# Kernel optimization log

Hardware: AMD Instinct MI355X
Metric: run time of the kernel (lower is better)

## Reference

```python
import jax, jax.numpy as jnp
import numpy as np

I, H, O = 8, 32, 1  # input_size, hidden_size, output_size


def setup_inputs() -> dict:
    key = jax.random.key(0)
    ks = jax.random.split(key, 7)
    B, T = 4096, 256
    s_ih = 1.0 / np.sqrt(H)
    inp = {
        "x": jax.random.normal(ks[0], (B, T, I), dtype=jnp.float32),
        # PyTorch nn.LSTM params, gate order [i, f, g, o]
        "W_ih": jax.random.uniform(ks[1], (4 * H, I), minval=-s_ih, maxval=s_ih, dtype=jnp.float32),
        "W_hh": jax.random.uniform(ks[2], (4 * H, H), minval=-s_ih, maxval=s_ih, dtype=jnp.float32),
        "b_ih": jax.random.uniform(ks[3], (4 * H,), minval=-s_ih, maxval=s_ih, dtype=jnp.float32),
        "b_hh": jax.random.uniform(ks[4], (4 * H,), minval=-s_ih, maxval=s_ih, dtype=jnp.float32),
        # nn.Linear(H, O)
        "W_out": jax.random.uniform(ks[5], (O, H), minval=-s_ih, maxval=s_ih, dtype=jnp.float32),
        "b_out": jax.random.uniform(ks[6], (O,), minval=-s_ih, maxval=s_ih, dtype=jnp.float32),
    }
    return inp


def _lstm_last_h(x, W_ih, W_hh, b_ih, b_hh):
    B = x.shape[0]
    # Precompute input projections for all steps: [T, B, 4H]
    x_proj = jnp.einsum("bti,gi->tbg", x, W_ih) + (b_ih + b_hh)
    h0 = jnp.zeros((B, H), dtype=x.dtype)
    c0 = jnp.zeros((B, H), dtype=x.dtype)

    def step(carry, xp):
        h, c = carry
        z = xp + h @ W_hh.T  # [B, 4H]
        i = jax.nn.sigmoid(z[:, 0 * H:1 * H])
        f = jax.nn.sigmoid(z[:, 1 * H:2 * H])
        g = jnp.tanh(z[:, 2 * H:3 * H])
        o = jax.nn.sigmoid(z[:, 3 * H:4 * H])
        c = f * c + i * g
        h = o * jnp.tanh(c)
        return (h, c), None

    (hT, _), _ = jax.lax.scan(step, (h0, c0), x_proj)
    return hT  # equals out[:, -1, :] for unidirectional batch_first LSTM


def reference(x, W_ih, W_hh, b_ih, b_hh, W_out, b_out):
    hT = _lstm_last_h(x, W_ih, W_hh, b_ih, b_hh)
    return hT @ W_out.T + b_out  # [B, O]
```

## Files before the change

### kernel.cpp

```cpp
#include <hip/hip_runtime.h>


#define T_LEN   256
#define HALF_T  128
#define XSTRIDE 130
#define LOG2E   1.4426950408889634f

typedef short bf16x8 __attribute__((ext_vector_type(8)));
typedef float f32x4  __attribute__((ext_vector_type(4)));
typedef unsigned u32x4 __attribute__((ext_vector_type(4)));

static __device__ inline short f2bf_rne(float f) {
    union { float f; unsigned u; } v; v.f = f;
    unsigned u = v.u;
    return (short)((u + 0x7FFFu + ((u >> 16) & 1u)) >> 16);
}
static __device__ inline unsigned pack_bf2(float a, float b) {
    union { float f; unsigned u; } x, y; x.f = a; y.f = b;
    return ((x.u + 0x8000u) >> 16) | ((y.u + 0x8000u) & 0xFFFF0000u);
}
static __device__ inline float bf2f(short s) {
    union { unsigned u; float f; } v;
    v.u = ((unsigned)(unsigned short)s) << 16;
    return v.f;
}

__global__ __launch_bounds__(256) void lstm_kernel(
    const float* __restrict__ x, const float* __restrict__ W_ih,
    const float* __restrict__ W_hh, const float* __restrict__ b_ih,
    const float* __restrict__ b_hh, const float* __restrict__ W_out,
    const float* __restrict__ b_out, float* __restrict__ out)
{
    __shared__ __attribute__((aligned(16))) short xl[HALF_T * XSTRIDE];
    __shared__ __attribute__((aligned(16))) short h_lds[2][16 * 40];

    const int tid  = threadIdx.x;
    const int w    = tid >> 6;
    const int lane = tid & 63;
    const int L    = lane & 15;
    const int q    = lane >> 4;
    const int row0 = blockIdx.x * 16;
    const float4* xv = (const float4*)x;

    bf16x8 whh[2], wih[2];
    f32x4  bias[2];
#pragma unroll
    for (int e = 0; e < 2; ++e) {
        const int   n = 32 * (L & 3) + 8 * (L >> 2) + 2 * w + e;
        const float s = ((L & 3) == 2 ? 2.f * LOG2E : LOG2E);
        const float* src = W_hh + n * 32 + q * 8;
        bf16x8 fr;
#pragma unroll
        for (int j = 0; j < 8; ++j) fr[j] = f2bf_rne(src[j] * s);
        whh[e] = fr;
        bf16x8 gr = (bf16x8){0,0,0,0,0,0,0,0};
        if (q == 0) {
            const float* s2 = W_ih + n * 8;
#pragma unroll
            for (int j = 0; j < 8; ++j) gr[j] = f2bf_rne(s2[j] * s);
        }
        wih[e] = gr;
        f32x4 bb;
#pragma unroll
        for (int r = 0; r < 4; ++r) {
            const int   nr = 32 * r + 8 * q + 2 * w + e;
            const float sr = (r == 2 ? 2.f * LOG2E : LOG2E);
            bb[r] = (b_ih[nr] + b_hh[nr]) * sr;
        }
        bias[e] = bb;
    }

    for (int i = tid; i < 16 * 40; i += 256) h_lds[0][i] = 0;

#pragma unroll
    for (int it = 0; it < 8; ++it) {
        const int idx = tid + (it << 8);
        const int L2  = idx >> 7;
        const int tl  = idx & (HALF_T - 1);
        const float4* srcp = xv + ((size_t)(row0 + L2) * T_LEN + tl) * 2;
        const float4 a = srcp[0], b = srcp[1];
        u32x4 u;
        u[0] = pack_bf2(a.x, a.y); u[1] = pack_bf2(a.z, a.w);
        u[2] = pack_bf2(b.x, b.y); u[3] = pack_bf2(b.z, b.w);
        *(u32x4*)(&xl[tl * XSTRIDE + L2 * 8]) = u;
    }
    __syncthreads();

    f32x4 zx[2];
    {
        const bf16x8 xf0 = *(const bf16x8*)(&xl[L * 8]);
        zx[0] = __builtin_amdgcn_mfma_f32_16x16x32_bf16(wih[0], xf0, bias[0], 0, 0, 0);
        zx[1] = __builtin_amdgcn_mfma_f32_16x16x32_bf16(wih[1], xf0, bias[1], 0, 0, 0);
    }

    float c0 = 0.f, c1 = 0.f;

#pragma unroll 2
    for (int t = 0; t < T_LEN; ++t) {
        if (t == HALF_T - 1) {
#pragma unroll
            for (int it = 0; it < 8; ++it) {
                const int idx = tid + (it << 8);
                const int L2  = idx >> 7;
                const int tl  = idx & (HALF_T - 1);
                const float4* srcp = xv + ((size_t)(row0 + L2) * T_LEN + HALF_T + tl) * 2;
                const float4 a = srcp[0], b = srcp[1];
                u32x4 u;
                u[0] = pack_bf2(a.x, a.y); u[1] = pack_bf2(a.z, a.w);
                u[2] = pack_bf2(b.x, b.y); u[3] = pack_bf2(b.z, b.w);
                *(u32x4*)(&xl[tl * XSTRIDE + L2 * 8]) = u;
            }
            __syncthreads();
        }

        const int par = t & 1, nxt = par ^ 1;

        const bf16x8 hfrag = *(const bf16x8*)(&h_lds[par][L * 40 + q * 8]);
        int tn = t + 1; if (tn >= T_LEN) tn = T_LEN - 1;
        const bf16x8 xfrag = *(const bf16x8*)(&xl[(tn & (HALF_T - 1)) * XSTRIDE + L * 8]);

        const f32x4 a0 = __builtin_amdgcn_mfma_f32_16x16x32_bf16(whh[0], hfrag, zx[0], 0, 0, 0);
        const f32x4 a1 = __builtin_amdgcn_mfma_f32_16x16x32_bf16(whh[1], hfrag, zx[1], 0, 0, 0);
        zx[0] = __builtin_amdgcn_mfma_f32_16x16x32_bf16(wih[0], xfrag, bias[0], 0, 0, 0);
        zx[1] = __builtin_amdgcn_mfma_f32_16x16x32_bf16(wih[1], xfrag, bias[1], 0, 0, 0);

        float h0, h1;
        {
            const float ei = __builtin_amdgcn_exp2f(-a0[0]);
            const float ef = __builtin_amdgcn_exp2f(-a0[1]);
            const float eg = __builtin_amdgcn_exp2f(-a0[2]);
            const float eo = __builtin_amdgcn_exp2f(-a0[3]);
            const float fv = __builtin_amdgcn_rcpf(1.f + ef);
            const float ig = (1.f - eg) * __builtin_amdgcn_rcpf((1.f + ei) * (1.f + eg));
            c0 = fmaf(fv, c0, ig);
            const float ec = __builtin_amdgcn_exp2f(fminf(c0 * (-2.f * LOG2E), 40.f));
            h0 = (1.f - ec) * __builtin_amdgcn_rcpf((1.f + eo) * (1.f + ec));
        }
        {
            const float ei = __builtin_amdgcn_exp2f(-a1[0]);
            const float ef = __builtin_amdgcn_exp2f(-a1[1]);
            const float eg = __builtin_amdgcn_exp2f(-a1[2]);
            const float eo = __builtin_amdgcn_exp2f(-a1[3]);
            const float fv = __builtin_amdgcn_rcpf(1.f + ef);
            const float ig = (1.f - eg) * __builtin_amdgcn_rcpf((1.f + ei) * (1.f + eg));
            c1 = fmaf(fv, c1, ig);
            const float ec = __builtin_amdgcn_exp2f(fminf(c1 * (-2.f * LOG2E), 40.f));
            h1 = (1.f - ec) * __builtin_amdgcn_rcpf((1.f + eo) * (1.f + ec));
        }

        *(unsigned*)(&h_lds[nxt][L * 40 + 8 * q + 2 * w]) = pack_bf2(h0, h1);

        __syncthreads();
    }

    if (tid < 16) {
        float s = b_out[0];
#pragma unroll
        for (int k = 0; k < 32; ++k) s = fmaf(bf2f(h_lds[0][tid * 40 + k]), W_out[k], s);
        out[row0 + tid] = s;
    }
}

extern "C" void kernel_launch(void* const* d_in, const int* in_sizes, int n_in,
                              void* d_out, int out_size, void* d_ws, size_t ws_size,
                              hipStream_t stream) {
    const float* x     = (const float*)d_in[0];
    const float* W_ih  = (const float*)d_in[1];
    const float* W_hh  = (const float*)d_in[2];
    const float* b_ih  = (const float*)d_in[3];
    const float* b_hh  = (const float*)d_in[4];
    const float* W_out = (const float*)d_in[5];
    const float* b_out = (const float*)d_in[6];
    float* out = (float*)d_out;

    const int B = in_sizes[0] / (T_LEN * 8);
    const int tiles = B / 16;
    lstm_kernel<<<tiles, 256, 0, stream>>>(x, W_ih, W_hh, b_ih, b_hh, W_out, b_out, out);
}
```

Baseline: 147.8 us.

## Run each batch tile on a single wave with register-resident hidden state

Collapses the four-wave block into one 64-lane wave that computes all 128 gate rows via eight MFMAs per step. The MFMA output layout is reused directly as the next step's hidden-state operand, removing the per-step LDS round trip and block barrier. Input x is streamed from global memory with a small register prefetch ring instead of being staged in LDS. The trade-off is four times more serial gate arithmetic per wave and lower occupancy per CU.

```diff
diff --git a/kernel.cpp b/kernel.cpp
--- a/kernel.cpp
+++ b/kernel.cpp
@@ -1,10 +1,8 @@
 #include <hip/hip_runtime.h>
 
 
-#define T_LEN   256
-#define HALF_T  128
-#define XSTRIDE 130
-#define LOG2E   1.4426950408889634f
+#define T_LEN 256
+#define LOG2E 1.4426950408889634f
 
 typedef short bf16x8 __attribute__((ext_vector_type(8)));
 typedef float f32x4  __attribute__((ext_vector_type(4)));
@@ -19,146 +17,120 @@
     union { float f; unsigned u; } x, y; x.f = a; y.f = b;
     return ((x.u + 0x8000u) >> 16) | ((y.u + 0x8000u) & 0xFFFF0000u);
 }
-static __device__ inline float bf2f(short s) {
-    union { unsigned u; float f; } v;
-    v.u = ((unsigned)(unsigned short)s) << 16;
-    return v.f;
-}
 
-__global__ __launch_bounds__(256) void lstm_kernel(
+__global__ __launch_bounds__(64, 1) void lstm_kernel(
     const float* __restrict__ x, const float* __restrict__ W_ih,
     const float* __restrict__ W_hh, const float* __restrict__ b_ih,
     const float* __restrict__ b_hh, const float* __restrict__ W_out,
     const float* __restrict__ b_out, float* __restrict__ out)
 {
-    __shared__ __attribute__((aligned(16))) short xl[HALF_T * XSTRIDE];
-    __shared__ __attribute__((aligned(16))) short h_lds[2][16 * 40];
-
-    const int tid  = threadIdx.x;
-    const int w    = tid >> 6;
-    const int lane = tid & 63;
+    const int lane = threadIdx.x;
     const int L    = lane & 15;
     const int q    = lane >> 4;
     const int row0 = blockIdx.x * 16;
-    const float4* xv = (const float4*)x;
 
-    bf16x8 whh[2], wih[2];
-    f32x4  bias[2];
+    const int   nbase = 32 * (L & 3) + 8 * (L >> 2);
+    const float sc    = ((L & 3) == 2 ? 2.f * LOG2E : LOG2E);
+    bf16x8 whh[8], wih[8];
+    f32x4  bias[8];
 #pragma unroll
-    for (int e = 0; e < 2; ++e) {
-        const int   n = 32 * (L & 3) + 8 * (L >> 2) + 2 * w + e;
-        const float s = ((L & 3) == 2 ? 2.f * LOG2E : LOG2E);
+    for (int k = 0; k < 8; ++k) {
+        const int n = nbase + k;
         const float* src = W_hh + n * 32 + q * 8;
         bf16x8 fr;
 #pragma unroll
-        for (int j = 0; j < 8; ++j) fr[j] = f2bf_rne(src[j] * s);
-        whh[e] = fr;
+        for (int j = 0; j < 8; ++j) fr[j] = f2bf_rne(src[j] * sc);
+        whh[k] = fr;
         bf16x8 gr = (bf16x8){0,0,0,0,0,0,0,0};
         if (q == 0) {
             const float* s2 = W_ih + n * 8;
 #pragma unroll
-            for (int j = 0; j < 8; ++j) gr[j] = f2bf_rne(s2[j] * s);
+            for (int j = 0; j < 8; ++j) gr[j] = f2bf_rne(s2[j] * sc);
         }
-        wih[e] = gr;
+        wih[k] = gr;
         f32x4 bb;
 #pragma unroll
         for (int r = 0; r < 4; ++r) {
-            const int   nr = 32 * r + 8 * q + 2 * w + e;
+            const int   nr = 32 * r + 8 * q + k;
             const float sr = (r == 2 ? 2.f * LOG2E : LOG2E);
             bb[r] = (b_ih[nr] + b_hh[nr]) * sr;
         }
-        bias[e] = bb;
+        bias[k] = bb;
     }
 
-    for (int i = tid; i < 16 * 40; i += 256) h_lds[0][i] = 0;
+    const float4* xv = (const float4*)x;
+    const size_t  xb = (size_t)(row0 + L) * (T_LEN * 8 / 4);
+    float4 r0[4], r1[4];
+    const float4 a0 = xv[xb + 0], b0 = xv[xb + 1];
+    r0[1] = xv[xb + 2]; r1[1] = xv[xb + 3];
+    r0[2] = xv[xb + 4]; r1[2] = xv[xb + 5];
+    r0[3] = xv[xb + 6]; r1[3] = xv[xb + 7];
+    r0[0] = xv[xb + 8]; r1[0] = xv[xb + 9];
+
+    f32x4 zx[8];
+    {
+        u32x4 u;
+        u[0] = pack_bf2(a0.x, a0.y); u[1] = pack_bf2(a0.z, a0.w);
+        u[2] = pack_bf2(b0.x, b0.y); u[3] = pack_bf2(b0.z, b0.w);
+        const bf16x8 xf0 = *(const bf16x8*)&u;
+#pragma unroll
+        for (int k = 0; k < 8; ++k)
+            zx[k] = __builtin_amdgcn_mfma_f32_16x16x32_bf16(wih[k], xf0, bias[k], 0, 0, 0);
+    }
+
+    bf16x8 hfrag = (bf16x8){0,0,0,0,0,0,0,0};
+    float c[8]  = {0,0,0,0,0,0,0,0};
+    float hh[8] = {0,0,0,0,0,0,0,0};
+
+#pragma unroll 4
+    for (int t = 0; t < T_LEN; ++t) {
+        f32x4 acc[8];
+#pragma unroll
+        for (int k = 0; k < 8; ++k)
+            acc[k] = __builtin_amdgcn_mfma_f32_16x16x32_bf16(whh[k], hfrag, zx[k], 0, 0, 0);
+
+        {
+            const int s = (t + 1) & 3;
+            const float4 a = r0[s], b = r1[s];
+            u32x4 u;
+            u[0] = pack_bf2(a.x, a.y); u[1] = pack_bf2(a.z, a.w);
+            u[2] = pack_bf2(b.x, b.y); u[3] = pack_bf2(b.z, b.w);
+            const bf16x8 xf = *(const bf16x8*)&u;
+            int tn = t + 5; if (tn >= T_LEN) tn = T_LEN - 1;
+            r0[s] = xv[xb + (size_t)tn * 2];
+            r1[s] = xv[xb + (size_t)tn * 2 + 1];
+#pragma unroll
+            for (int k = 0; k < 8; ++k)
+                zx[k] = __builtin_amdgcn_mfma_f32_16x16x32_bf16(wih[k], xf, bias[k], 0, 0, 0);
+        }
 
 #pragma unroll
-    for (int it = 0; it < 8; ++it) {
-        const int idx = tid + (it << 8);
-        const int L2  = idx >> 7;
-        const int tl  = idx & (HALF_T - 1);
-        const float4* srcp = xv + ((size_t)(row0 + L2) * T_LEN + tl) * 2;
-        const float4 a = srcp[0], b = srcp[1];
-        u32x4 u;
-        u[0] = pack_bf2(a.x, a.y); u[1] = pack_bf2(a.z, a.w);
-        u[2] = pack_bf2(b.x, b.y); u[3] = pack_bf2(b.z, b.w);
-        *(u32x4*)(&xl[tl * XSTRIDE + L2 * 8]) = u;
-    }
-    __syncthreads();
+        for (int k = 0; k < 8; ++k) {
+            const float ei = __builtin_amdgcn_exp2f(-acc[k][0]);
+            const float ef = __builtin_amdgcn_exp2f(-acc[k][1]);
+            const float eg = __builtin_amdgcn_exp2f(-acc[k][2]);
+            const float eo = __builtin_amdgcn_exp2f(-acc[k][3]);
+            const float fv = __builtin_amdgcn_rcpf(1.f + ef);
+            const float ig = (1.f - eg) * __builtin_amdgcn_rcpf((1.f + ei) * (1.f + eg));
+            c[k] = fmaf(fv, c[k], ig);
+            const float ec = __builtin_amdgcn_exp2f(fminf(c[k] * (-2.f * LOG2E), 40.f));
+            hh[k] = (1.f - ec) * __builtin_amdgcn_rcpf((1.f + eo) * (1.f + ec));
+        }
 
-    f32x4 zx[2];
-    {
-        const bf16x8 xf0 = *(const bf16x8*)(&xl[L * 8]);
-        zx[0] = __builtin_amdgcn_mfma_f32_16x16x32_bf16(wih[0], xf0, bias[0], 0, 0, 0);
-        zx[1] = __builtin_amdgcn_mfma_f32_16x16x32_bf16(wih[1], xf0, bias[1], 0, 0, 0);
+        {
+            u32x4 hu;
+            hu[0] = pack_bf2(hh[0], hh[1]); hu[1] = pack_bf2(hh[2], hh[3]);
+            hu[2] = pack_bf2(hh[4], hh[5]); hu[3] = pack_bf2(hh[6], hh[7]);
+            hfrag = *(const bf16x8*)&hu;
+        }
     }
 
-    float c0 = 0.f, c1 = 0.f;
-
-#pragma unroll 2
-    for (int t = 0; t < T_LEN; ++t) {
-        if (t == HALF_T - 1) {
+    float s = 0.f;
 #pragma unroll
-            for (int it = 0; it < 8; ++it) {
-                const int idx = tid + (it << 8);
-                const int L2  = idx >> 7;
-                const int tl  = idx & (HALF_T - 1);
-                const float4* srcp = xv + ((size_t)(row0 + L2) * T_LEN + HALF_T + tl) * 2;
-                const float4 a = srcp[0], b = srcp[1];
-                u32x4 u;
-                u[0] = pack_bf2(a.x, a.y); u[1] = pack_bf2(a.z, a.w);
-                u[2] = pack_bf2(b.x, b.y); u[3] = pack_bf2(b.z, b.w);
-                *(u32x4*)(&xl[tl * XSTRIDE + L2 * 8]) = u;
-            }
-            __syncthreads();
-        }
-
-        const int par = t & 1, nxt = par ^ 1;
-
-        const bf16x8 hfrag = *(const bf16x8*)(&h_lds[par][L * 40 + q * 8]);
-        int tn = t + 1; if (tn >= T_LEN) tn = T_LEN - 1;
-        const bf16x8 xfrag = *(const bf16x8*)(&xl[(tn & (HALF_T - 1)) * XSTRIDE + L * 8]);
-
-        const f32x4 a0 = __builtin_amdgcn_mfma_f32_16x16x32_bf16(whh[0], hfrag, zx[0], 0, 0, 0);
-        const f32x4 a1 = __builtin_amdgcn_mfma_f32_16x16x32_bf16(whh[1], hfrag, zx[1], 0, 0, 0);
-        zx[0] = __builtin_amdgcn_mfma_f32_16x16x32_bf16(wih[0], xfrag, bias[0], 0, 0, 0);
-        zx[1] = __builtin_amdgcn_mfma_f32_16x16x32_bf16(wih[1], xfrag, bias[1], 0, 0, 0);
-
-        float h0, h1;
-        {
-            const float ei = __builtin_amdgcn_exp2f(-a0[0]);
-            const float ef = __builtin_amdgcn_exp2f(-a0[1]);
-            const float eg = __builtin_amdgcn_exp2f(-a0[2]);
-            const float eo = __builtin_amdgcn_exp2f(-a0[3]);
-            const float fv = __builtin_amdgcn_rcpf(1.f + ef);
-            const float ig = (1.f - eg) * __builtin_amdgcn_rcpf((1.f + ei) * (1.f + eg));
-            c0 = fmaf(fv, c0, ig);
-            const float ec = __builtin_amdgcn_exp2f(fminf(c0 * (-2.f * LOG2E), 40.f));
-            h0 = (1.f - ec) * __builtin_amdgcn_rcpf((1.f + eo) * (1.f + ec));
-        }
-        {
-            const float ei = __builtin_amdgcn_exp2f(-a1[0]);
-            const float ef = __builtin_amdgcn_exp2f(-a1[1]);
-            const float eg = __builtin_amdgcn_exp2f(-a1[2]);
-            const float eo = __builtin_amdgcn_exp2f(-a1[3]);
-            const float fv = __builtin_amdgcn_rcpf(1.f + ef);
-            const float ig = (1.f - eg) * __builtin_amdgcn_rcpf((1.f + ei) * (1.f + eg));
-            c1 = fmaf(fv, c1, ig);
-            const float ec = __builtin_amdgcn_exp2f(fminf(c1 * (-2.f * LOG2E), 40.f));
-            h1 = (1.f - ec) * __builtin_amdgcn_rcpf((1.f + eo) * (1.f + ec));
-        }
-
-        *(unsigned*)(&h_lds[nxt][L * 40 + 8 * q + 2 * w]) = pack_bf2(h0, h1);
-
-        __syncthreads();
-    }
-
-    if (tid < 16) {
-        float s = b_out[0];
-#pragma unroll
-        for (int k = 0; k < 32; ++k) s = fmaf(bf2f(h_lds[0][tid * 40 + k]), W_out[k], s);
-        out[row0 + tid] = s;
-    }
+    for (int k = 0; k < 8; ++k) s += hh[k] * W_out[8 * q + k];
+    s += __shfl_xor(s, 16, 64);
+    s += __shfl_xor(s, 32, 64);
+    if (lane < 16) out[row0 + L] = s + b_out[0];
 }
 
 extern "C" void kernel_launch(void* const* d_in, const int* in_sizes, int n_in,
@@ -175,5 +147,5 @@
 
     const int B = in_sizes[0] / (T_LEN * 8);
     const int tiles = B / 16;
-    lstm_kernel<<<tiles, 256, 0, stream>>>(x, W_ih, W_hh, b_ih, b_hh, W_out, b_out, out);
+    lstm_kernel<<<tiles, 64, 0, stream>>>(x, W_ih, W_hh, b_ih, b_hh, W_out, b_out, out);
 }
```

Result: slower. 238.1 us (+61.1%).

## Split LSTM gate work across 8 waves with one MFMA tile per wave

Applied to the files above, without the earlier changes.

Doubles the block to 512 threads so each of 8 waves owns one 16-column gate tile instead of two. Per step each wave now issues one recurrent MFMA and one input MFMA and evaluates a single set of activations, which shortens the serial per-step critical path. The cost is more waves per block joining the per-step barrier, and hidden-state writes become 16-bit stores instead of packed 32-bit stores.

```diff
diff --git a/kernel.cpp b/kernel.cpp
--- a/kernel.cpp
+++ b/kernel.cpp
@@ -15,6 +15,10 @@
     unsigned u = v.u;
     return (short)((u + 0x7FFFu + ((u >> 16) & 1u)) >> 16);
 }
+static __device__ inline short f2bf_fast(float f) {
+    union { float f; unsigned u; } v; v.f = f;
+    return (short)((v.u + 0x8000u) >> 16);
+}
 static __device__ inline unsigned pack_bf2(float a, float b) {
     union { float f; unsigned u; } x, y; x.f = a; y.f = b;
     return ((x.u + 0x8000u) >> 16) | ((y.u + 0x8000u) & 0xFFFF0000u);
@@ -25,7 +29,7 @@
     return v.f;
 }
 
-__global__ __launch_bounds__(256) void lstm_kernel(
+__global__ __launch_bounds__(512, 2) void lstm_kernel(
     const float* __restrict__ x, const float* __restrict__ W_ih,
     const float* __restrict__ W_hh, const float* __restrict__ b_ih,
     const float* __restrict__ b_hh, const float* __restrict__ W_out,
@@ -42,39 +46,32 @@
     const int row0 = blockIdx.x * 16;
     const float4* xv = (const float4*)x;
 
-    bf16x8 whh[2], wih[2];
-    f32x4  bias[2];
+    const int   n  = 32 * (L & 3) + 4 * w + (L >> 2);
+    const float sc = ((L & 3) == 2 ? 2.f * LOG2E : LOG2E);
+    bf16x8 whh_f, wih_f = (bf16x8){0,0,0,0,0,0,0,0};
+    {
+        const float* src = W_hh + n * 32 + q * 8;
 #pragma unroll
-    for (int e = 0; e < 2; ++e) {
-        const int   n = 32 * (L & 3) + 8 * (L >> 2) + 2 * w + e;
-        const float s = ((L & 3) == 2 ? 2.f * LOG2E : LOG2E);
-        const float* src = W_hh + n * 32 + q * 8;
-        bf16x8 fr;
-#pragma unroll
-        for (int j = 0; j < 8; ++j) fr[j] = f2bf_rne(src[j] * s);
-        whh[e] = fr;
-        bf16x8 gr = (bf16x8){0,0,0,0,0,0,0,0};
+        for (int j = 0; j < 8; ++j) whh_f[j] = f2bf_rne(src[j] * sc);
         if (q == 0) {
             const float* s2 = W_ih + n * 8;
 #pragma unroll
-            for (int j = 0; j < 8; ++j) gr[j] = f2bf_rne(s2[j] * s);
+            for (int j = 0; j < 8; ++j) wih_f[j] = f2bf_rne(s2[j] * sc);
         }
-        wih[e] = gr;
-        f32x4 bb;
+    }
+    f32x4 bias;
 #pragma unroll
-        for (int r = 0; r < 4; ++r) {
-            const int   nr = 32 * r + 8 * q + 2 * w + e;
-            const float sr = (r == 2 ? 2.f * LOG2E : LOG2E);
-            bb[r] = (b_ih[nr] + b_hh[nr]) * sr;
-        }
-        bias[e] = bb;
+    for (int r = 0; r < 4; ++r) {
+        const int   nr = 32 * r + 4 * w + q;
+        const float sr = (r == 2 ? 2.f * LOG2E : LOG2E);
+        bias[r] = (b_ih[nr] + b_hh[nr]) * sr;
     }
 
-    for (int i = tid; i < 16 * 40; i += 256) h_lds[0][i] = 0;
+    for (int i = tid; i < 16 * 40; i += 512) h_lds[0][i] = 0;
 
 #pragma unroll
-    for (int it = 0; it < 8; ++it) {
-        const int idx = tid + (it << 8);
+    for (int it = 0; it < 4; ++it) {
+        const int idx = tid + (it << 9);
         const int L2  = idx >> 7;
         const int tl  = idx & (HALF_T - 1);
         const float4* srcp = xv + ((size_t)(row0 + L2) * T_LEN + tl) * 2;
@@ -86,21 +83,21 @@
     }
     __syncthreads();
 
-    f32x4 zx[2];
+    f32x4 zx;
     {
         const bf16x8 xf0 = *(const bf16x8*)(&xl[L * 8]);
-        zx[0] = __builtin_amdgcn_mfma_f32_16x16x32_bf16(wih[0], xf0, bias[0], 0, 0, 0);
-        zx[1] = __builtin_amdgcn_mfma_f32_16x16x32_bf16(wih[1], xf0, bias[1], 0, 0, 0);
+        zx = __builtin_amdgcn_mfma_f32_16x16x32_bf16(wih_f, xf0, bias, 0, 0, 0);
     }
 
-    float c0 = 0.f, c1 = 0.f;
+    float c = 0.f;
+    const int hw_off = 4 * w + q;
 
 #pragma unroll 2
     for (int t = 0; t < T_LEN; ++t) {
         if (t == HALF_T - 1) {
 #pragma unroll
-            for (int it = 0; it < 8; ++it) {
-                const int idx = tid + (it << 8);
+            for (int it = 0; it < 4; ++it) {
+                const int idx = tid + (it << 9);
                 const int L2  = idx >> 7;
                 const int tl  = idx & (HALF_T - 1);
                 const float4* srcp = xv + ((size_t)(row0 + L2) * T_LEN + HALF_T + tl) * 2;
@@ -119,36 +116,21 @@
         int tn = t + 1; if (tn >= T_LEN) tn = T_LEN - 1;
         const bf16x8 xfrag = *(const bf16x8*)(&xl[(tn & (HALF_T - 1)) * XSTRIDE + L * 8]);
 
-        const f32x4 a0 = __builtin_amdgcn_mfma_f32_16x16x32_bf16(whh[0], hfrag, zx[0], 0, 0, 0);
-        const f32x4 a1 = __builtin_amdgcn_mfma_f32_16x16x32_bf16(whh[1], hfrag, zx[1], 0, 0, 0);
-        zx[0] = __builtin_amdgcn_mfma_f32_16x16x32_bf16(wih[0], xfrag, bias[0], 0, 0, 0);
-        zx[1] = __builtin_amdgcn_mfma_f32_16x16x32_bf16(wih[1], xfrag, bias[1], 0, 0, 0);
+        const f32x4 acc = __builtin_amdgcn_mfma_f32_16x16x32_bf16(whh_f, hfrag, zx, 0, 0, 0);
+        zx = __builtin_amdgcn_mfma_f32_16x16x32_bf16(wih_f, xfrag, bias, 0, 0, 0);
 
-        float h0, h1;
         {
-            const float ei = __builtin_amdgcn_exp2f(-a0[0]);
-            const float ef = __builtin_amdgcn_exp2f(-a0[1]);
-            const float eg = __builtin_amdgcn_exp2f(-a0[2]);
-            const float eo = __builtin_amdgcn_exp2f(-a0[3]);
+            const float ei = __builtin_amdgcn_exp2f(-acc[0]);
+            const float ef = __builtin_amdgcn_exp2f(-acc[1]);
+            const float eg = __builtin_amdgcn_exp2f(-acc[2]);
+            const float eo = __builtin_amdgcn_exp2f(-acc[3]);
             const float fv = __builtin_amdgcn_rcpf(1.f + ef);
             const float ig = (1.f - eg) * __builtin_amdgcn_rcpf((1.f + ei) * (1.f + eg));
-            c0 = fmaf(fv, c0, ig);
-            const float ec = __builtin_amdgcn_exp2f(fminf(c0 * (-2.f * LOG2E), 40.f));
-            h0 = (1.f - ec) * __builtin_amdgcn_rcpf((1.f + eo) * (1.f + ec));
+            c = fmaf(fv, c, ig);
+            const float ec = __builtin_amdgcn_exp2f(fminf(c * (-2.f * LOG2E), 40.f));
+            const float hv = (1.f - ec) * __builtin_amdgcn_rcpf((1.f + eo) * (1.f + ec));
+            h_lds[nxt][L * 40 + hw_off] = f2bf_fast(hv);
         }
-        {
-            const float ei = __builtin_amdgcn_exp2f(-a1[0]);
-            const float ef = __builtin_amdgcn_exp2f(-a1[1]);
-            const float eg = __builtin_amdgcn_exp2f(-a1[2]);
-            const float eo = __builtin_amdgcn_exp2f(-a1[3]);
-            const float fv = __builtin_amdgcn_rcpf(1.f + ef);
-            const float ig = (1.f - eg) * __builtin_amdgcn_rcpf((1.f + ei) * (1.f + eg));
-            c1 = fmaf(fv, c1, ig);
-            const float ec = __builtin_amdgcn_exp2f(fminf(c1 * (-2.f * LOG2E), 40.f));
-            h1 = (1.f - ec) * __builtin_amdgcn_rcpf((1.f + eo) * (1.f + ec));
-        }
-
-        *(unsigned*)(&h_lds[nxt][L * 40 + 8 * q + 2 * w]) = pack_bf2(h0, h1);
 
         __syncthreads();
     }
@@ -175,5 +157,5 @@
 
     const int B = in_sizes[0] / (T_LEN * 8);
     const int tiles = B / 16;
-    lstm_kernel<<<tiles, 256, 0, stream>>>(x, W_ih, W_hh, b_ih, b_hh, W_out, b_out, out);
+    lstm_kernel<<<tiles, 512, 0, stream>>>(x, W_ih, W_hh, b_ih, b_hh, W_out, b_out, out);
 }
```

New measurement: 141.4 us. 4.4% less time.

## Stagger two batch-row groups per block to overlap MFMA with gate activations

Applied to the files above, without the earlier changes.

Each block now handles 32 batch rows as two 16-row groups of 4 waves. The groups run the recurrence half a step out of phase, so one group issues the recurrent MFMAs while the other evaluates the gate nonlinearities, with a block-wide barrier between half-steps. The input sequence is staged into LDS in 64-step chunks per group instead of two 128-step halves. The aim is to hide MFMA and transcendental latency, at the cost of twice as many barriers, larger blocks, and half as many blocks in the grid, which may leave many CUs idle.

```diff
diff --git a/kernel.cpp b/kernel.cpp
--- a/kernel.cpp
+++ b/kernel.cpp
@@ -2,7 +2,7 @@
 
 
 #define T_LEN   256
-#define HALF_T  128
+#define CH      64
 #define XSTRIDE 130
 #define LOG2E   1.4426950408889634f
 
@@ -25,139 +25,149 @@
     return v.f;
 }
 
-__global__ __launch_bounds__(256) void lstm_kernel(
+__global__ __launch_bounds__(512, 2) void lstm_kernel(
     const float* __restrict__ x, const float* __restrict__ W_ih,
     const float* __restrict__ W_hh, const float* __restrict__ b_ih,
     const float* __restrict__ b_hh, const float* __restrict__ W_out,
     const float* __restrict__ b_out, float* __restrict__ out)
 {
-    __shared__ __attribute__((aligned(16))) short xl[HALF_T * XSTRIDE];
-    __shared__ __attribute__((aligned(16))) short h_lds[2][16 * 40];
+    __shared__ __attribute__((aligned(16))) short xl[2][CH * XSTRIDE];
+    __shared__ __attribute__((aligned(16))) short h_lds[2][2][16 * 40];
 
-    const int tid  = threadIdx.x;
-    const int w    = tid >> 6;
-    const int lane = tid & 63;
-    const int L    = lane & 15;
-    const int q    = lane >> 4;
-    const int row0 = blockIdx.x * 16;
+    const int tid   = threadIdx.x;
+    const int w     = tid >> 6;
+    const int grp   = w >> 2;
+    const int w4    = w & 3;
+    const int lane  = tid & 63;
+    const int L     = lane & 15;
+    const int q     = lane >> 4;
+    const int rbase = blockIdx.x * 32 + grp * 16;
+    const int ttid  = tid & 255;
     const float4* xv = (const float4*)x;
 
     bf16x8 whh[2], wih[2];
     f32x4  bias[2];
 #pragma unroll
     for (int e = 0; e < 2; ++e) {
-        const int   n = 32 * (L & 3) + 8 * (L >> 2) + 2 * w + e;
-        const float s = ((L & 3) == 2 ? 2.f * LOG2E : LOG2E);
+        const int   n  = 32 * (L & 3) + 8 * (L >> 2) + 2 * w4 + e;
+        const float sc = ((L & 3) == 2 ? 2.f * LOG2E : LOG2E);
         const float* src = W_hh + n * 32 + q * 8;
         bf16x8 fr;
 #pragma unroll
-        for (int j = 0; j < 8; ++j) fr[j] = f2bf_rne(src[j] * s);
+        for (int j = 0; j < 8; ++j) fr[j] = f2bf_rne(src[j] * sc);
         whh[e] = fr;
         bf16x8 gr = (bf16x8){0,0,0,0,0,0,0,0};
         if (q == 0) {
             const float* s2 = W_ih + n * 8;
 #pragma unroll
-            for (int j = 0; j < 8; ++j) gr[j] = f2bf_rne(s2[j] * s);
+            for (int j = 0; j < 8; ++j) gr[j] = f2bf_rne(s2[j] * sc);
         }
         wih[e] = gr;
         f32x4 bb;
 #pragma unroll
         for (int r = 0; r < 4; ++r) {
-            const int   nr = 32 * r + 8 * q + 2 * w + e;
+            const int   nr = 32 * r + 8 * q + 2 * w4 + e;
             const float sr = (r == 2 ? 2.f * LOG2E : LOG2E);
             bb[r] = (b_ih[nr] + b_hh[nr]) * sr;
         }
         bias[e] = bb;
     }
 
-    for (int i = tid; i < 16 * 40; i += 256) h_lds[0][i] = 0;
+    for (int i = tid; i < 2 * 2 * 16 * 40; i += 512) ((short*)h_lds)[i] = 0;
 
 #pragma unroll
-    for (int it = 0; it < 8; ++it) {
-        const int idx = tid + (it << 8);
-        const int L2  = idx >> 7;
-        const int tl  = idx & (HALF_T - 1);
-        const float4* srcp = xv + ((size_t)(row0 + L2) * T_LEN + tl) * 2;
+    for (int it = 0; it < 4; ++it) {
+        const int idx = ttid + (it << 8);
+        const int tl  = idx & (CH - 1);
+        const int L2  = idx >> 6;
+        const float4* srcp = xv + ((size_t)(rbase - grp * 16 + grp * 16 + L2) * T_LEN + tl) * 2;
         const float4 a = srcp[0], b = srcp[1];
         u32x4 u;
         u[0] = pack_bf2(a.x, a.y); u[1] = pack_bf2(a.z, a.w);
         u[2] = pack_bf2(b.x, b.y); u[3] = pack_bf2(b.z, b.w);
-        *(u32x4*)(&xl[tl * XSTRIDE + L2 * 8]) = u;
+        *(u32x4*)(&xl[grp][tl * XSTRIDE + L2 * 8]) = u;
     }
     __syncthreads();
 
     f32x4 zx[2];
     {
-        const bf16x8 xf0 = *(const bf16x8*)(&xl[L * 8]);
+        const bf16x8 xf0 = *(const bf16x8*)(&xl[grp][L * 8]);
         zx[0] = __builtin_amdgcn_mfma_f32_16x16x32_bf16(wih[0], xf0, bias[0], 0, 0, 0);
         zx[1] = __builtin_amdgcn_mfma_f32_16x16x32_bf16(wih[1], xf0, bias[1], 0, 0, 0);
     }
 
+    f32x4 acc0 = {0,0,0,0}, acc1 = {0,0,0,0};
     float c0 = 0.f, c1 = 0.f;
 
-#pragma unroll 2
-    for (int t = 0; t < T_LEN; ++t) {
-        if (t == HALF_T - 1) {
+    for (int ck = 0; ck < 4; ++ck) {
+        if (ck) {
 #pragma unroll
-            for (int it = 0; it < 8; ++it) {
-                const int idx = tid + (it << 8);
-                const int L2  = idx >> 7;
-                const int tl  = idx & (HALF_T - 1);
-                const float4* srcp = xv + ((size_t)(row0 + L2) * T_LEN + HALF_T + tl) * 2;
+            for (int it = 0; it < 4; ++it) {
+                const int idx = ttid + (it << 8);
+                const int tl  = idx & (CH - 1);
+                const int L2  = idx >> 6;
+                const float4* srcp = xv + ((size_t)(rbase + L2) * T_LEN + 64 * ck + tl) * 2;
                 const float4 a = srcp[0], b = srcp[1];
                 u32x4 u;
                 u[0] = pack_bf2(a.x, a.y); u[1] = pack_bf2(a.z, a.w);
                 u[2] = pack_bf2(b.x, b.y); u[3] = pack_bf2(b.z, b.w);
-                *(u32x4*)(&xl[tl * XSTRIDE + L2 * 8]) = u;
+                *(u32x4*)(&xl[grp][tl * XSTRIDE + L2 * 8]) = u;
             }
             __syncthreads();
         }
+        const int s0 = ck ? (128 * ck - 1) : 0;
+        const int s1 = (ck == 3) ? 512 : (128 * (ck + 1) - 2);
+        for (int s = s0; s <= s1; ++s) {
+            if (((s ^ grp) & 1) == 0) {
+                const int t = (s - grp) >> 1;
+                if (t < T_LEN) {
+                    const bf16x8 hfrag = *(const bf16x8*)(&h_lds[grp][t & 1][L * 40 + q * 8]);
+                    acc0 = __builtin_amdgcn_mfma_f32_16x16x32_bf16(whh[0], hfrag, zx[0], 0, 0, 0);
+                    acc1 = __builtin_amdgcn_mfma_f32_16x16x32_bf16(whh[1], hfrag, zx[1], 0, 0, 0);
+                }
+            } else {
+                const int t = (s - 1 - grp) >> 1;
+                if (t >= 0) {
+                    float h0, h1;
+                    {
+                        const float ei = __builtin_amdgcn_exp2f(-acc0[0]);
+                        const float ef = __builtin_amdgcn_exp2f(-acc0[1]);
+                        const float eg = __builtin_amdgcn_exp2f(-acc0[2]);
+                        const float eo = __builtin_amdgcn_exp2f(-acc0[3]);
+                        const float fv = __builtin_amdgcn_rcpf(1.f + ef);
+                        const float ig = (1.f - eg) * __builtin_amdgcn_rcpf((1.f + ei) * (1.f + eg));
+                        c0 = fmaf(fv, c0, ig);
+                        const float ec = __builtin_amdgcn_exp2f(fminf(c0 * (-2.f * LOG2E), 40.f));
+                        h0 = (1.f - ec) * __builtin_amdgcn_rcpf((1.f + eo) * (1.f + ec));
+                    }
+                    {
+                        const float ei = __builtin_amdgcn_exp2f(-acc1[0]);
+                        const float ef = __builtin_amdgcn_exp2f(-acc1[1]);
+                        const float eg = __builtin_amdgcn_exp2f(-acc1[2]);
+                        const float eo = __builtin_amdgcn_exp2f(-acc1[3]);
+                        const float fv = __builtin_amdgcn_rcpf(1.f + ef);
+                        const float ig = (1.f - eg) * __builtin_amdgcn_rcpf((1.f + ei) * (1.f + eg));
+                        c1 = fmaf(fv, c1, ig);
+                        const float ec = __builtin_amdgcn_exp2f(fminf(c1 * (-2.f * LOG2E), 40.f));
+                        h1 = (1.f - ec) * __builtin_amdgcn_rcpf((1.f + eo) * (1.f + ec));
+                    }
+                    *(unsigned*)(&h_lds[grp][(t + 1) & 1][L * 40 + 8 * q + 2 * w4]) = pack_bf2(h0, h1);
 
-        const int par = t & 1, nxt = par ^ 1;
-
-        const bf16x8 hfrag = *(const bf16x8*)(&h_lds[par][L * 40 + q * 8]);
-        int tn = t + 1; if (tn >= T_LEN) tn = T_LEN - 1;
-        const bf16x8 xfrag = *(const bf16x8*)(&xl[(tn & (HALF_T - 1)) * XSTRIDE + L * 8]);
-
-        const f32x4 a0 = __builtin_amdgcn_mfma_f32_16x16x32_bf16(whh[0], hfrag, zx[0], 0, 0, 0);
-        const f32x4 a1 = __builtin_amdgcn_mfma_f32_16x16x32_bf16(whh[1], hfrag, zx[1], 0, 0, 0);
-        zx[0] = __builtin_amdgcn_mfma_f32_16x16x32_bf16(wih[0], xfrag, bias[0], 0, 0, 0);
-        zx[1] = __builtin_amdgcn_mfma_f32_16x16x32_bf16(wih[1], xfrag, bias[1], 0, 0, 0);
-
-        float h0, h1;
-        {
-            const float ei = __builtin_amdgcn_exp2f(-a0[0]);
-            const float ef = __builtin_amdgcn_exp2f(-a0[1]);
-            const float eg = __builtin_amdgcn_exp2f(-a0[2]);
-            const float eo = __builtin_amdgcn_exp2f(-a0[3]);
-            const float fv = __builtin_amdgcn_rcpf(1.f + ef);
-            const float ig = (1.f - eg) * __builtin_amdgcn_rcpf((1.f + ei) * (1.f + eg));
-            c0 = fmaf(fv, c0, ig);
-            const float ec = __builtin_amdgcn_exp2f(fminf(c0 * (-2.f * LOG2E), 40.f));
-            h0 = (1.f - ec) * __builtin_amdgcn_rcpf((1.f + eo) * (1.f + ec));
+                    int tn = t + 1; if (tn >= T_LEN) tn = T_LEN - 1;
+                    const bf16x8 xfrag = *(const bf16x8*)(&xl[grp][(tn & (CH - 1)) * XSTRIDE + L * 8]);
+                    zx[0] = __builtin_amdgcn_mfma_f32_16x16x32_bf16(wih[0], xfrag, bias[0], 0, 0, 0);
+                    zx[1] = __builtin_amdgcn_mfma_f32_16x16x32_bf16(wih[1], xfrag, bias[1], 0, 0, 0);
+                }
+            }
+            __syncthreads();
         }
-        {
-            const float ei = __builtin_amdgcn_exp2f(-a1[0]);
-            const float ef = __builtin_amdgcn_exp2f(-a1[1]);
-            const float eg = __builtin_amdgcn_exp2f(-a1[2]);
-            const float eo = __builtin_amdgcn_exp2f(-a1[3]);
-            const float fv = __builtin_amdgcn_rcpf(1.f + ef);
-            const float ig = (1.f - eg) * __builtin_amdgcn_rcpf((1.f + ei) * (1.f + eg));
-            c1 = fmaf(fv, c1, ig);
-            const float ec = __builtin_amdgcn_exp2f(fminf(c1 * (-2.f * LOG2E), 40.f));
-            h1 = (1.f - ec) * __builtin_amdgcn_rcpf((1.f + eo) * (1.f + ec));
-        }
-
-        *(unsigned*)(&h_lds[nxt][L * 40 + 8 * q + 2 * w]) = pack_bf2(h0, h1);
-
-        __syncthreads();
     }
 
-    if (tid < 16) {
+    if (lane < 16 && w4 == 0) {
         float s = b_out[0];
 #pragma unroll
-        for (int k = 0; k < 32; ++k) s = fmaf(bf2f(h_lds[0][tid * 40 + k]), W_out[k], s);
-        out[row0 + tid] = s;
+        for (int k = 0; k < 32; ++k) s = fmaf(bf2f(h_lds[grp][0][L * 40 + k]), W_out[k], s);
+        out[rbase + L] = s;
     }
 }
 
@@ -174,6 +184,6 @@
     float* out = (float*)d_out;
 
     const int B = in_sizes[0] / (T_LEN * 8);
-    const int tiles = B / 16;
-    lstm_kernel<<<tiles, 256, 0, stream>>>(x, W_ih, W_hh, b_ih, b_hh, W_out, b_out, out);
+    const int blocks = B / 32;
+    lstm_kernel<<<blocks, 512, 0, stream>>>(x, W_ih, W_hh, b_ih, b_hh, W_out, b_out, out);
 }
```

New measurement: 233.3 us. +57.8%, slower.
